# Optimization experiments

Hardware: AMD Instinct MI355X
Metric: run time of the kernel (lower is better)

## Reference

```python
import jax, jax.numpy as jnp
import numpy as np

N_NODES = 50000
N_EDGES = 800000
D = 128
BN_EPS = 1e-5


def gcn_conv(x, src, dst, W, b, n_nodes):
    # x: [N, Din]; src/dst: [E+N] (self-loops already appended)
    h = x @ W  # [N, Dout]
    deg = jax.ops.segment_sum(jnp.ones_like(src, dtype=h.dtype), dst, num_segments=n_nodes)
    dinv = jnp.where(deg > 0, jax.lax.rsqrt(deg), 0.0)  # deg^{-1/2}
    norm = dinv[src] * dinv[dst]  # [E+N]
    msg = h[src] * norm[:, None]  # gather + scale
    out = jax.ops.segment_sum(msg, dst, num_segments=n_nodes)  # scatter-add
    return out + b


def batchnorm_prelu(x, gamma, beta, a):
    # training-mode BN over node dim (biased variance), then PReLU
    mu = jnp.mean(x, axis=0)
    var = jnp.mean(jnp.square(x - mu), axis=0)
    xn = (x - mu) * jax.lax.rsqrt(var + BN_EPS)
    y = xn * gamma + beta
    return jnp.where(y >= 0, y, a * y)


def setup_inputs():
    key = jax.random.key(0)
    ks = jax.random.split(key, 8)
    x = jax.random.normal(ks[0], (N_NODES, D), dtype=jnp.float32)
    edge_index = jax.random.randint(ks[1], (2, N_EDGES), 0, N_NODES, dtype=jnp.int32)
    lim = float(np.sqrt(6.0 / (D + D)))  # glorot
    W1 = jax.random.uniform(ks[2], (D, D), jnp.float32, -lim, lim)
    W2 = jax.random.uniform(ks[3], (D, D), jnp.float32, -lim, lim)
    b1 = jnp.zeros((D,), jnp.float32)
    b2 = jnp.zeros((D,), jnp.float32)
    gamma1 = jnp.ones((D,), jnp.float32)
    beta1 = jnp.zeros((D,), jnp.float32)
    gamma2 = jnp.ones((D,), jnp.float32)
    beta2 = jnp.zeros((D,), jnp.float32)
    a1 = jnp.full((1,), 0.25, jnp.float32)
    a2 = jnp.full((1,), 0.25, jnp.float32)
    return {"x": x, "edge_index": edge_index, "W1": W1, "b1": b1, "gamma1": gamma1,
            "beta1": beta1, "a1": a1, "W2": W2, "b2": b2, "gamma2": gamma2,
            "beta2": beta2, "a2": a2}


def reference(x, edge_index, W1, b1, gamma1, beta1, a1, W2, b2, gamma2, beta2, a2):
    n = x.shape[0]
    loops = jnp.arange(n, dtype=edge_index.dtype)
    src = jnp.concatenate([edge_index[0], loops])
    dst = jnp.concatenate([edge_index[1], loops])
    h = gcn_conv(x, src, dst, W1, b1, n)
    h = batchnorm_prelu(h, gamma1, beta1, a1)
    h = gcn_conv(h, src, dst, W2, b2, n)
    h = batchnorm_prelu(h, gamma2, beta2, a2)
    return h
```

## Files before the change

### kernel.cpp

```cpp
#include <hip/hip_runtime.h>
#include <hip/hip_bf16.h>

#define N_NODES 50000
#define N_EDGES 800000
#define D 128
#define BN_EPS 1e-5f
#define GEMM_ROWS 128
#define LDS_PITCH 136

#define BSH 8
#define NB 196
#define TILE 4096
#define NTILES ((N_EDGES + TILE - 1) / TILE)
#define REC_CAP 6144
#define CSR_CHUNKS (REC_CAP / 256)

typedef unsigned short u16;
typedef short bf16x8 __attribute__((ext_vector_type(8)));
typedef float f32x4  __attribute__((ext_vector_type(4)));

__device__ __forceinline__ u16 f2bf(float f) {
    union { float f; unsigned int u; } v; v.f = f;
    unsigned int u = v.u;
    return (u16)((u + 0x7FFF + ((u >> 16) & 1)) >> 16);
}
__device__ __forceinline__ float bflo(unsigned int u) {
    union { unsigned int u; float f; } v; v.u = u << 16; return v.f;
}
__device__ __forceinline__ float bfhi(unsigned int u) {
    union { unsigned int u; float f; } v; v.u = u & 0xFFFF0000u; return v.f;
}
__device__ __forceinline__ unsigned int packbf(float a, float b) {
    return (unsigned int)f2bf(a) | ((unsigned int)f2bf(b) << 16);
}

__global__ __launch_bounds__(256) void hist_prep(const int* __restrict__ dst,
                                                 const float* __restrict__ W1,
                                                 const float* __restrict__ W2,
                                                 int* __restrict__ thist,
                                                 u16* __restrict__ Wt1,
                                                 u16* __restrict__ Wt2,
                                                 float* __restrict__ sums) {
    __shared__ int h[256];
    const int t = threadIdx.x;
    const int b = blockIdx.x;
    if (b < NTILES) {
        h[t] = 0;
        __syncthreads();
        const int e0 = b * TILE;
#pragma unroll
        for (int i = 0; i < 16; ++i) {
            int e = e0 + t + 256 * i;
            if (e < N_EDGES) atomicAdd(&h[dst[e] >> BSH], 1);
        }
        __syncthreads();
        thist[b * 256 + t] = h[t];
    } else {
        const int wb = b - NTILES;
        if (wb == 0) { sums[t] = 0.f; sums[256 + t] = 0.f; }
        int u = wb * 256 + t;
        const float* W = (u < 16384) ? W1 : W2;
        u16* Wt        = (u < 16384) ? Wt1 : Wt2;
        int v = u & 16383;
        int k = v >> 7, n = v & 127;
        Wt[n * 128 + k] = f2bf(W[v]);
    }
}

template <bool BN_IN>
__device__ __forceinline__ void gemm_body(const void* __restrict__ Xv,
                                          const u16* __restrict__ Wt,
                                          u16* __restrict__ C,
                                          const float* __restrict__ sums,
                                          const float* __restrict__ gamma,
                                          const float* __restrict__ beta,
                                          const float* __restrict__ a,
                                          int nrows, int row0,
                                          u16* __restrict__ As,
                                          u16* __restrict__ Ws) {
    const int tid  = threadIdx.x;
    const float invN = 1.0f / (float)N_NODES;

    const bf16x8* Wt8 = (const bf16x8*)Wt;
#pragma unroll
    for (int i = 0; i < 8; ++i) {
        int u = tid + 256 * i;
        int n = u >> 4, kg = u & 15;
        *(bf16x8*)&Ws[n * LDS_PITCH + kg * 8] = Wt8[u];
    }

    if (BN_IN) {
        const uint4* X4 = (const uint4*)Xv;
        const float av = a[0];
#pragma unroll
        for (int i = 0; i < 8; ++i) {
            int u    = tid + 256 * i;
            int r    = u >> 4, kg = u & 15;
            int grow = row0 + r;
            uint4 o = make_uint4(0, 0, 0, 0);
            if (grow < nrows) {
                uint4 v = X4[(size_t)grow * 16 + kg];
                float f[8] = { bflo(v.x), bfhi(v.x), bflo(v.y), bfhi(v.y),
                               bflo(v.z), bfhi(v.z), bflo(v.w), bfhi(v.w) };
#pragma unroll
                for (int c = 0; c < 8; ++c) {
                    int fe     = kg * 8 + c;
                    float mean = sums[fe] * invN;
                    float var  = sums[128 + fe] * invN - mean * mean;
                    float sc   = rsqrtf(var + BN_EPS) * gamma[fe];
                    float y    = (f[c] - mean) * sc + beta[fe];
                    f[c]       = (y >= 0.f) ? y : av * y;
                }
                o.x = packbf(f[0], f[1]); o.y = packbf(f[2], f[3]);
                o.z = packbf(f[4], f[5]); o.w = packbf(f[6], f[7]);
            }
            *(uint4*)&As[r * LDS_PITCH + kg * 8] = o;
        }
    } else {
        const float4* X4 = (const float4*)Xv;
#pragma unroll
        for (int i = 0; i < 16; ++i) {
            int u    = tid + 256 * i;
            int r    = u >> 5, kf = u & 31;
            int grow = row0 + r;
            float4 v = make_float4(0.f, 0.f, 0.f, 0.f);
            if (grow < nrows) v = X4[(size_t)grow * 32 + kf];
            ushort4 p;
            p.x = f2bf(v.x); p.y = f2bf(v.y); p.z = f2bf(v.z); p.w = f2bf(v.w);
            *(ushort4*)&As[r * LDS_PITCH + kf * 4] = p;
        }
    }
    __syncthreads();

    const int wv   = tid >> 6;
    const int lane = tid & 63;
    const int n    = lane & 15;
    const int q    = lane >> 4;
    const int c0   = wv * 32;

    bf16x8 bfr[4][2];
#pragma unroll
    for (int kb = 0; kb < 4; ++kb)
#pragma unroll
        for (int c = 0; c < 2; ++c)
            bfr[kb][c] = *(const bf16x8*)&Ws[(c0 + 16 * c + n) * LDS_PITCH + 32 * kb + 8 * q];

    f32x4 acc[8][2];
    const f32x4 z = {0.f, 0.f, 0.f, 0.f};
#pragma unroll
    for (int rt = 0; rt < 8; ++rt) { acc[rt][0] = z; acc[rt][1] = z; }

#pragma unroll
    for (int kb = 0; kb < 4; ++kb) {
#pragma unroll
        for (int rt = 0; rt < 8; ++rt) {
            bf16x8 af = *(const bf16x8*)&As[(16 * rt + n) * LDS_PITCH + 32 * kb + 8 * q];
            acc[rt][0] = __builtin_amdgcn_mfma_f32_16x16x32_bf16(af, bfr[kb][0], acc[rt][0], 0, 0, 0);
            acc[rt][1] = __builtin_amdgcn_mfma_f32_16x16x32_bf16(af, bfr[kb][1], acc[rt][1], 0, 0, 0);
        }
    }

#pragma unroll
    for (int rt = 0; rt < 8; ++rt) {
        int gr0 = row0 + 16 * rt + 4 * q;
#pragma unroll
        for (int r = 0; r < 4; ++r) {
            int gr = gr0 + r;
            if (gr < nrows) {
                C[(size_t)gr * D + c0 + n]      = f2bf(acc[rt][0][r]);
                C[(size_t)gr * D + c0 + 16 + n] = f2bf(acc[rt][1][r]);
            }
        }
    }
}

__device__ __forceinline__ unsigned long long match8(int key, bool valid) {
    unsigned long long vm = __ballot(valid ? 1 : 0);
    unsigned long long m  = ~0ull;
#pragma unroll
    for (int bit = 0; bit < 8; ++bit) {
        unsigned long long vb = __ballot((key >> bit) & 1);
        m &= ((key >> bit) & 1) ? vb : ~vb;
    }
    return m & vm;
}

__global__ __launch_bounds__(256) void scatter_gemm1(const int* __restrict__ src,
                                                     const int* __restrict__ dst,
                                                     const int* __restrict__ thist,
                                                     unsigned int* __restrict__ brec,
                                                     int* __restrict__ btot,
                                                     int* __restrict__ bbase,
                                                     int* __restrict__ row_ptr,
                                                     const float* __restrict__ x,
                                                     const u16* __restrict__ Wt1,
                                                     u16* __restrict__ C) {
    __shared__ __align__(16) u16 smem[2 * 128 * LDS_PITCH];

    if (blockIdx.x >= NTILES) {
        gemm_body<false>(x, Wt1, C, nullptr, nullptr, nullptr, nullptr,
                         N_NODES, (int)(blockIdx.x - NTILES) * GEMM_ROWS,
                         smem, smem + 128 * LDS_PITCH);
        return;
    }

    int* wcnt  = (int*)smem;
    int* sb    = wcnt + 4 * 256;
    int* lbase = sb + 256;
    int* gbase = lbase + 256;
    unsigned int*  rec = (unsigned int*)(gbase + 256);
    unsigned char* rbk = (unsigned char*)(rec + TILE);

    const int tile = blockIdx.x;
    const int t    = threadIdx.x;
    const int lane = t & 63;
    const int w    = t >> 6;
    const int e0   = tile * TILE;
    const int tcount = min(TILE, N_EDGES - e0);
    const unsigned long long lt = (1ull << lane) - 1ull;

    wcnt[t] = 0; wcnt[256 + t] = 0; wcnt[512 + t] = 0; wcnt[768 + t] = 0;
    __syncthreads();

    unsigned int myrec[16];
    int          myb[16];
    int          myrank[16];
#pragma unroll
    for (int i = 0; i < 16; ++i) {
        int e = e0 + t + 256 * i;
        bool valid = (e < N_EDGES);
        unsigned int s_ = 0, d_ = 0;
        if (valid) { s_ = (unsigned int)src[e]; d_ = (unsigned int)dst[e]; }
        int b = valid ? (int)(d_ >> BSH) : 0;
        myb[i]   = valid ? b : -1;
        myrec[i] = s_ | ((d_ & 255u) << 16);
        unsigned long long m = match8(b, valid);
        int pre  = __popcll(m & lt);
        int base = wcnt[w * 256 + b];
        myrank[i] = base + pre;
        if (valid && pre == 0) wcnt[w * 256 + b] = base + __popcll(m);
    }
    __syncthreads();

    int c0 = wcnt[t], c1 = wcnt[256 + t], c2 = wcnt[512 + t], c3 = wcnt[768 + t];
    int tot_l = c0 + c1 + c2 + c3;
    wcnt[t] = 0; wcnt[256 + t] = c0; wcnt[512 + t] = c0 + c1; wcnt[768 + t] = c0 + c1 + c2;
    sb[t] = tot_l;
    __syncthreads();
#pragma unroll
    for (int off = 1; off < 256; off <<= 1) {
        int add = (t >= off) ? sb[t - off] : 0;
        __syncthreads();
        sb[t] += add;
        __syncthreads();
    }
    lbase[t] = sb[t] - tot_l;
    __syncthreads();

#pragma unroll
    for (int i = 0; i < 16; ++i) {
        if (myb[i] >= 0) {
            int p = lbase[myb[i]] + wcnt[w * 256 + myb[i]] + myrank[i];
            rec[p] = myrec[i];
            rbk[p] = (unsigned char)myb[i];
        }
    }

    int tot = 0, pre = 0;
    for (int j = 0; j < NTILES; ++j) {
        int v = thist[j * 256 + t];
        tot += v;
        if (j < tile) pre += v;
    }
    __syncthreads();
    sb[t] = tot;
    __syncthreads();
#pragma unroll
    for (int off = 1; off < 256; off <<= 1) {
        int add = (t >= off) ? sb[t - off] : 0;
        __syncthreads();
        sb[t] += add;
        __syncthreads();
    }
    int bb = sb[t] - tot;
    gbase[t] = bb + pre;
    if (tile == NTILES - 1 && t < NB) {
        btot[t]  = tot;
        bbase[t] = bb;
        if (t == 0) row_ptr[N_NODES] = N_EDGES;
    }
    __syncthreads();

    for (int i = t; i < tcount; i += 256) {
        int b = rbk[i];
        brec[gbase[b] + (i - lbase[b])] = rec[i];
    }
}

__global__ __launch_bounds__(256) void bucket_csr(const unsigned int* __restrict__ brec,
                                                  const int* __restrict__ bbase,
                                                  const int* __restrict__ btot,
                                                  int* __restrict__ row_ptr,
                                                  u16* __restrict__ col,
                                                  float* __restrict__ dinv) {
    __shared__ unsigned int rec[REC_CAP];
    __shared__ u16 cls[REC_CAP];
    __shared__ int wcnt[4 * 256];
    __shared__ int sb[256];
    __shared__ int lb[256];
    const int b    = blockIdx.x;
    const int t    = threadIdx.x;
    const int lane = t & 63;
    const int w    = t >> 6;
    const int base = bbase[b];
    const int cnt  = min(btot[b], REC_CAP);
    const int n0   = b << BSH;
    const int nn   = min(256, N_NODES - n0);
    const unsigned long long lt = (1ull << lane) - 1ull;

    for (int i = t; i < cnt; i += 256) rec[i] = brec[base + i];
    wcnt[t] = 0; wcnt[256 + t] = 0; wcnt[512 + t] = 0; wcnt[768 + t] = 0;
    __syncthreads();

    int myrank[CSR_CHUNKS];
#pragma unroll
    for (int kk = 0; kk < CSR_CHUNKS; ++kk) {
        int i = t + 256 * kk;
        bool valid = (i < cnt);
        int c = valid ? (int)((rec[i] >> 16) & 255u) : 0;
        unsigned long long m = match8(c, valid);
        int pre  = __popcll(m & lt);
        int bs_  = wcnt[w * 256 + c];
        myrank[kk] = bs_ + pre;
        if (valid && pre == 0) wcnt[w * 256 + c] = bs_ + __popcll(m);
    }
    __syncthreads();

    int c0 = wcnt[t], c1 = wcnt[256 + t], c2 = wcnt[512 + t], c3 = wcnt[768 + t];
    int tot = c0 + c1 + c2 + c3;
    wcnt[t] = 0; wcnt[256 + t] = c0; wcnt[512 + t] = c0 + c1; wcnt[768 + t] = c0 + c1 + c2;
    sb[t] = tot;
    __syncthreads();
#pragma unroll
    for (int off = 1; off < 256; off <<= 1) {
        int add = (t >= off) ? sb[t - off] : 0;
        __syncthreads();
        sb[t] += add;
        __syncthreads();
    }
    int excl = sb[t] - tot;
    lb[t] = excl;
    if (t < nn) {
        row_ptr[n0 + t] = base + excl;
        dinv[n0 + t]    = rsqrtf((float)tot + 1.0f);
    }
    __syncthreads();

#pragma unroll
    for (int kk = 0; kk < CSR_CHUNKS; ++kk) {
        int i = t + 256 * kk;
        if (i < cnt) {
            unsigned int r = rec[i];
            int c = (int)((r >> 16) & 255u);
            int p = lb[c] + wcnt[w * 256 + c] + myrank[kk];
            cls[p] = (u16)(r & 0xFFFFu);
        }
    }
    __syncthreads();
    for (int i = t; i < cnt; i += 256) col[base + i] = cls[i];
}

__global__ __launch_bounds__(256) void gemm2_k(const u16* __restrict__ Obf,
                                               const u16* __restrict__ Wt2,
                                               u16* __restrict__ C,
                                               const float* __restrict__ sums,
                                               const float* __restrict__ gamma,
                                               const float* __restrict__ beta,
                                               const float* __restrict__ a) {
    __shared__ __align__(16) u16 smem[2 * 128 * LDS_PITCH];
    gemm_body<true>(Obf, Wt2, C, sums, gamma, beta, a,
                    N_NODES, (int)blockIdx.x * GEMM_ROWS,
                    smem, smem + 128 * LDS_PITCH);
}

__global__ __launch_bounds__(256, 4) void pull_agg_bn(const u16* __restrict__ H,
                                                      const int* __restrict__ row_ptr,
                                                      const u16* __restrict__ col,
                                                      const float* __restrict__ dinv,
                                                      u16* __restrict__ out,
                                                      float* __restrict__ sums) {
    const int sub = threadIdx.x & 15;
    const int d   = (blockIdx.x * 256 + threadIdx.x) >> 4;
    const uint4* H4   = (const uint4*)H;
    uint4*       out4 = (uint4*)out;

    const int beg = row_ptr[d];
    const int end = row_ptr[d + 1];
    const float dv = dinv[d];
    float a0[8], a1[8] = {};
    {
        uint4 v = H4[(size_t)d * 16 + sub];
        a0[0] = dv * bflo(v.x); a0[1] = dv * bfhi(v.x);
        a0[2] = dv * bflo(v.y); a0[3] = dv * bfhi(v.y);
        a0[4] = dv * bflo(v.z); a0[5] = dv * bfhi(v.z);
        a0[6] = dv * bflo(v.w); a0[7] = dv * bfhi(v.w);
    }
    for (int j = beg; j < end; j += 8) {
        int   s[8];
        float dd[8];
        uint4 w[8];
#pragma unroll
        for (int k = 0; k < 8; ++k) {
            int jj = j + k;
            int jc = (jj < end) ? jj : (end - 1);
            s[k] = (int)col[jc];
        }
#pragma unroll
        for (int k = 0; k < 8; ++k) {
            float dk = dinv[s[k]];
            dd[k] = (j + k < end) ? dk : 0.f;
        }
#pragma unroll
        for (int k = 0; k < 8; ++k) w[k] = H4[(size_t)s[k] * 16 + sub];
#pragma unroll
        for (int k = 0; k < 8; k += 2) {
            a0[0] += dd[k] * bflo(w[k].x); a0[1] += dd[k] * bfhi(w[k].x);
            a0[2] += dd[k] * bflo(w[k].y); a0[3] += dd[k] * bfhi(w[k].y);
            a0[4] += dd[k] * bflo(w[k].z); a0[5] += dd[k] * bfhi(w[k].z);
            a0[6] += dd[k] * bflo(w[k].w); a0[7] += dd[k] * bfhi(w[k].w);
            a1[0] += dd[k + 1] * bflo(w[k + 1].x); a1[1] += dd[k + 1] * bfhi(w[k + 1].x);
            a1[2] += dd[k + 1] * bflo(w[k + 1].y); a1[3] += dd[k + 1] * bfhi(w[k + 1].y);
            a1[4] += dd[k + 1] * bflo(w[k + 1].z); a1[5] += dd[k + 1] * bfhi(w[k + 1].z);
            a1[6] += dd[k + 1] * bflo(w[k + 1].w); a1[7] += dd[k + 1] * bfhi(w[k + 1].w);
        }
    }
    float r[8];
#pragma unroll
    for (int c = 0; c < 8; ++c) r[c] = (a0[c] + a1[c]) * dv;
    uint4 o;
    o.x = packbf(r[0], r[1]); o.y = packbf(r[2], r[3]);
    o.z = packbf(r[4], r[5]); o.w = packbf(r[6], r[7]);
    out4[(size_t)d * 16 + sub] = o;

    float bs[8], bq[8];
#pragma unroll
    for (int c = 0; c < 8; ++c) { bs[c] = r[c]; bq[c] = r[c] * r[c]; }
#pragma unroll
    for (int c = 0; c < 8; ++c) {
        bs[c] += __shfl_xor(bs[c], 16, 64);
        bs[c] += __shfl_xor(bs[c], 32, 64);
        bq[c] += __shfl_xor(bq[c], 16, 64);
        bq[c] += __shfl_xor(bq[c], 32, 64);
    }

    __shared__ float ls[4 * 256];
    const int lane = threadIdx.x & 63;
    const int wv   = threadIdx.x >> 6;
    if (lane < 16) {
#pragma unroll
        for (int c = 0; c < 8; ++c) {
            ls[wv * 256 + lane * 16 + c]     = bs[c];
            ls[wv * 256 + lane * 16 + 8 + c] = bq[c];
        }
    }
    __syncthreads();

    const int s2 = threadIdx.x >> 4;
    const int vi = threadIdx.x & 15;
    float v = ((ls[s2 * 16 + vi] + ls[256 + s2 * 16 + vi]) +
               (ls[512 + s2 * 16 + vi] + ls[768 + s2 * 16 + vi]));
    const int f = s2 * 8 + (vi & 7);
    atomicAdd(&sums[(vi < 8) ? f : (128 + f)], v);
}

__global__ void bn_prelu_bf(const u16* __restrict__ X, const float* __restrict__ sums,
                            const float* __restrict__ gamma, const float* __restrict__ beta,
                            const float* __restrict__ a, float* __restrict__ out,
                            float invN) {
    int idx = blockIdx.x * blockDim.x + threadIdx.x;
    if (idx >= N_NODES * 64) return;
    unsigned int u = ((const unsigned int*)X)[idx];
    int f0 = (idx * 2) & 127;
    float av = a[0];
    float2 o;
    {
        float mean = sums[f0] * invN;
        float var  = sums[128 + f0] * invN - mean * mean;
        float sc   = rsqrtf(var + BN_EPS) * gamma[f0];
        float y    = (bflo(u) - mean) * sc + beta[f0];
        o.x = (y >= 0.f) ? y : av * y;
    }
    {
        int f1 = f0 + 1;
        float mean = sums[f1] * invN;
        float var  = sums[128 + f1] * invN - mean * mean;
        float sc   = rsqrtf(var + BN_EPS) * gamma[f1];
        float y    = (bfhi(u) - mean) * sc + beta[f1];
        o.y = (y >= 0.f) ? y : av * y;
    }
    ((float2*)out)[idx] = o;
}

extern "C" void kernel_launch(void* const* d_in, const int* in_sizes, int n_in,
                              void* d_out, int out_size, void* d_ws, size_t ws_size,
                              hipStream_t stream) {
    const float* x      = (const float*)d_in[0];
    const int*   edges  = (const int*)d_in[1];
    const float* W1     = (const float*)d_in[2];
    const float* gamma1 = (const float*)d_in[4];
    const float* beta1  = (const float*)d_in[5];
    const float* a1     = (const float*)d_in[6];
    const float* W2     = (const float*)d_in[7];
    const float* gamma2 = (const float*)d_in[9];
    const float* beta2  = (const float*)d_in[10];
    const float* a2     = (const float*)d_in[11];

    const int* src = edges;
    const int* dst = edges + N_EDGES;

    float* OUT = (float*)d_out;
    char* ws = (char*)d_ws;
    u16*   Abf      = (u16*)ws;    ws += (size_t)N_NODES * D * sizeof(u16);
    u16*   Obf      = (u16*)ws;    ws += (size_t)N_NODES * D * sizeof(u16);
    float* dinv     = (float*)ws;  ws += N_NODES * sizeof(float);
    float* sums     = (float*)ws;  ws += 512 * sizeof(float);
    int*   row_ptr  = (int*)ws;    ws += (N_NODES + 1) * sizeof(int);
    int*   btot     = (int*)ws;    ws += NB * sizeof(int);
    int*   bbase    = (int*)ws;    ws += NB * sizeof(int);
    int*   thist    = (int*)ws;    ws += (size_t)NTILES * 256 * sizeof(int);
    unsigned int* brec = (unsigned int*)ws; ws += (size_t)N_EDGES * sizeof(unsigned int);
    u16*   col      = (u16*)ws;    ws += (size_t)N_EDGES * sizeof(u16);
    u16*   Wt1      = (u16*)ws;    ws += 16384 * sizeof(u16);
    u16*   Wt2      = (u16*)ws;    ws += 16384 * sizeof(u16);

    const float invN = 1.0f / (float)N_NODES;
    const int gemmGrid = (N_NODES + GEMM_ROWS - 1) / GEMM_ROWS;
    const int pullGrid = (N_NODES * 16) / 256;
    const int prGrid   = (N_NODES * 64 + 255) / 256;

    hist_prep<<<NTILES + 128, 256, 0, stream>>>(dst, W1, W2, thist, Wt1, Wt2, sums);

    scatter_gemm1<<<NTILES + gemmGrid, 256, 0, stream>>>(src, dst, thist, brec,
                                                         btot, bbase, row_ptr,
                                                         x, Wt1, Abf);
    bucket_csr<<<NB, 256, 0, stream>>>(brec, bbase, btot, row_ptr, col, dinv);

    pull_agg_bn<<<pullGrid, 256, 0, stream>>>(Abf, row_ptr, col, dinv, Obf, sums);

    gemm2_k<<<gemmGrid, 256, 0, stream>>>(Obf, Wt2, Abf, sums, gamma1, beta1, a1);
    pull_agg_bn<<<pullGrid, 256, 0, stream>>>(Abf, row_ptr, col, dinv, Obf, sums + 256);
    bn_prelu_bf<<<prGrid, 256, 0, stream>>>(Obf, sums + 256, gamma2, beta2, a2, OUT, invN);
}
```

Baseline: 344.3 us.

## Assign one wavefront per node in pull aggregation with grid-stride loop

The pull aggregation kernel now gives each destination node a full 64-lane wavefront instead of a 16-lane group. The four 16-lane slots split that node's edges, and their partial sums are combined with cross-lane shuffles. A persistent grid of 2048 blocks strides over the nodes and keeps BN sum and sum-of-squares in registers across iterations, so the block-level reduction and atomics happen once per block instead of once per 16 nodes. This is meant to give more memory parallelism per node and far fewer atomics. The cost is that lanes sit idle at the tail of low-degree rows, and all four slots do the self-loop load and the final math redundantly.

```diff
diff --git a/kernel.cpp b/kernel.cpp
--- a/kernel.cpp
+++ b/kernel.cpp
@@ -389,73 +389,81 @@
                                                       const float* __restrict__ dinv,
                                                       u16* __restrict__ out,
                                                       float* __restrict__ sums) {
-    const int sub = threadIdx.x & 15;
-    const int d   = (blockIdx.x * 256 + threadIdx.x) >> 4;
+    const int lane = threadIdx.x & 63;
+    const int wv   = threadIdx.x >> 6;
+    const int sub  = lane & 15;
+    const int slot = lane >> 4;
+    const int gw   = blockIdx.x * 4 + wv;
+    const int nw   = gridDim.x * 4;
     const uint4* H4   = (const uint4*)H;
     uint4*       out4 = (uint4*)out;
 
-    const int beg = row_ptr[d];
-    const int end = row_ptr[d + 1];
-    const float dv = dinv[d];
-    float a0[8], a1[8] = {};
-    {
-        uint4 v = H4[(size_t)d * 16 + sub];
-        a0[0] = dv * bflo(v.x); a0[1] = dv * bfhi(v.x);
-        a0[2] = dv * bflo(v.y); a0[3] = dv * bfhi(v.y);
-        a0[4] = dv * bflo(v.z); a0[5] = dv * bfhi(v.z);
-        a0[6] = dv * bflo(v.w); a0[7] = dv * bfhi(v.w);
-    }
-    for (int j = beg; j < end; j += 8) {
-        int   s[8];
-        float dd[8];
-        uint4 w[8];
-#pragma unroll
-        for (int k = 0; k < 8; ++k) {
-            int jj = j + k;
-            int jc = (jj < end) ? jj : (end - 1);
-            s[k] = (int)col[jc];
-        }
-#pragma unroll
-        for (int k = 0; k < 8; ++k) {
-            float dk = dinv[s[k]];
-            dd[k] = (j + k < end) ? dk : 0.f;
-        }
-#pragma unroll
-        for (int k = 0; k < 8; ++k) w[k] = H4[(size_t)s[k] * 16 + sub];
-#pragma unroll
-        for (int k = 0; k < 8; k += 2) {
-            a0[0] += dd[k] * bflo(w[k].x); a0[1] += dd[k] * bfhi(w[k].x);
-            a0[2] += dd[k] * bflo(w[k].y); a0[3] += dd[k] * bfhi(w[k].y);
-            a0[4] += dd[k] * bflo(w[k].z); a0[5] += dd[k] * bfhi(w[k].z);
-            a0[6] += dd[k] * bflo(w[k].w); a0[7] += dd[k] * bfhi(w[k].w);
-            a1[0] += dd[k + 1] * bflo(w[k + 1].x); a1[1] += dd[k + 1] * bfhi(w[k + 1].x);
-            a1[2] += dd[k + 1] * bflo(w[k + 1].y); a1[3] += dd[k + 1] * bfhi(w[k + 1].y);
-            a1[4] += dd[k + 1] * bflo(w[k + 1].z); a1[5] += dd[k + 1] * bfhi(w[k + 1].z);
-            a1[6] += dd[k + 1] * bflo(w[k + 1].w); a1[7] += dd[k + 1] * bfhi(w[k + 1].w);
-        }
-    }
-    float r[8];
-#pragma unroll
-    for (int c = 0; c < 8; ++c) r[c] = (a0[c] + a1[c]) * dv;
-    uint4 o;
-    o.x = packbf(r[0], r[1]); o.y = packbf(r[2], r[3]);
-    o.z = packbf(r[4], r[5]); o.w = packbf(r[6], r[7]);
-    out4[(size_t)d * 16 + sub] = o;
-
-    float bs[8], bq[8];
-#pragma unroll
-    for (int c = 0; c < 8; ++c) { bs[c] = r[c]; bq[c] = r[c] * r[c]; }
-#pragma unroll
-    for (int c = 0; c < 8; ++c) {
-        bs[c] += __shfl_xor(bs[c], 16, 64);
-        bs[c] += __shfl_xor(bs[c], 32, 64);
-        bq[c] += __shfl_xor(bq[c], 16, 64);
-        bq[c] += __shfl_xor(bq[c], 32, 64);
+    float bs[8] = {0.f, 0.f, 0.f, 0.f, 0.f, 0.f, 0.f, 0.f};
+    float bq[8] = {0.f, 0.f, 0.f, 0.f, 0.f, 0.f, 0.f, 0.f};
+
+    for (int d = gw; d < N_NODES; d += nw) {
+        const int beg = row_ptr[d];
+        const int end = row_ptr[d + 1];
+        const float dv = dinv[d];
+        float a0[8] = {}, a1[8] = {};
+
+        for (int j = beg; j < end; j += 16) {
+            const int e1 = end - 1;
+            int jj0 = j + slot, jj1 = j + 4 + slot, jj2 = j + 8 + slot, jj3 = j + 12 + slot;
+            int s0 = (int)col[min(jj0, e1)];
+            int s1 = (int)col[min(jj1, e1)];
+            int s2 = (int)col[min(jj2, e1)];
+            int s3 = (int)col[min(jj3, e1)];
+            float d0 = (jj0 < end) ? dinv[s0] : 0.f;
+            float d1 = (jj1 < end) ? dinv[s1] : 0.f;
+            float d2 = (jj2 < end) ? dinv[s2] : 0.f;
+            float d3 = (jj3 < end) ? dinv[s3] : 0.f;
+            uint4 w0 = H4[(size_t)s0 * 16 + sub];
+            uint4 w1 = H4[(size_t)s1 * 16 + sub];
+            uint4 w2 = H4[(size_t)s2 * 16 + sub];
+            uint4 w3 = H4[(size_t)s3 * 16 + sub];
+            a0[0] += d0 * bflo(w0.x); a0[1] += d0 * bfhi(w0.x);
+            a0[2] += d0 * bflo(w0.y); a0[3] += d0 * bfhi(w0.y);
+            a0[4] += d0 * bflo(w0.z); a0[5] += d0 * bfhi(w0.z);
+            a0[6] += d0 * bflo(w0.w); a0[7] += d0 * bfhi(w0.w);
+            a1[0] += d1 * bflo(w1.x); a1[1] += d1 * bfhi(w1.x);
+            a1[2] += d1 * bflo(w1.y); a1[3] += d1 * bfhi(w1.y);
+            a1[4] += d1 * bflo(w1.z); a1[5] += d1 * bfhi(w1.z);
+            a1[6] += d1 * bflo(w1.w); a1[7] += d1 * bfhi(w1.w);
+            a0[0] += d2 * bflo(w2.x); a0[1] += d2 * bfhi(w2.x);
+            a0[2] += d2 * bflo(w2.y); a0[3] += d2 * bfhi(w2.y);
+            a0[4] += d2 * bflo(w2.z); a0[5] += d2 * bfhi(w2.z);
+            a0[6] += d2 * bflo(w2.w); a0[7] += d2 * bfhi(w2.w);
+            a1[0] += d3 * bflo(w3.x); a1[1] += d3 * bfhi(w3.x);
+            a1[2] += d3 * bflo(w3.y); a1[3] += d3 * bfhi(w3.y);
+            a1[4] += d3 * bflo(w3.z); a1[5] += d3 * bfhi(w3.z);
+            a1[6] += d3 * bflo(w3.w); a1[7] += d3 * bfhi(w3.w);
+        }
+
+        float r[8];
+#pragma unroll
+        for (int c = 0; c < 8; ++c) r[c] = a0[c] + a1[c];
+#pragma unroll
+        for (int c = 0; c < 8; ++c) {
+            r[c] += __shfl_xor(r[c], 16, 64);
+            r[c] += __shfl_xor(r[c], 32, 64);
+        }
+        uint4 hv = H4[(size_t)d * 16 + sub];
+        r[0] = (r[0] + dv * bflo(hv.x)) * dv; r[1] = (r[1] + dv * bfhi(hv.x)) * dv;
+        r[2] = (r[2] + dv * bflo(hv.y)) * dv; r[3] = (r[3] + dv * bfhi(hv.y)) * dv;
+        r[4] = (r[4] + dv * bflo(hv.z)) * dv; r[5] = (r[5] + dv * bfhi(hv.z)) * dv;
+        r[6] = (r[6] + dv * bflo(hv.w)) * dv; r[7] = (r[7] + dv * bfhi(hv.w)) * dv;
+        if (slot == 0) {
+            uint4 o;
+            o.x = packbf(r[0], r[1]); o.y = packbf(r[2], r[3]);
+            o.z = packbf(r[4], r[5]); o.w = packbf(r[6], r[7]);
+            out4[(size_t)d * 16 + sub] = o;
+        }
+#pragma unroll
+        for (int c = 0; c < 8; ++c) { bs[c] += r[c]; bq[c] += r[c] * r[c]; }
     }
 
     __shared__ float ls[4 * 256];
-    const int lane = threadIdx.x & 63;
-    const int wv   = threadIdx.x >> 6;
     if (lane < 16) {
 #pragma unroll
         for (int c = 0; c < 8; ++c) {
@@ -535,7 +543,7 @@
 
     const float invN = 1.0f / (float)N_NODES;
     const int gemmGrid = (N_NODES + GEMM_ROWS - 1) / GEMM_ROWS;
-    const int pullGrid = (N_NODES * 16) / 256;
+    const int pullGrid = 2048;
     const int prGrid   = (N_NODES * 64 + 255) / 256;
 
     hist_prep<<<NTILES + 128, 256, 0, stream>>>(dst, W1, W2, thist, Wt1, Wt2, sums);
```

Result: faster. 311.1 us (-9.7%).
